# Kernel tuning notes

Hardware: AMD Instinct MI355X
Metric: run time of the kernel (lower is better)

The kernel has to match this reference:

```python
import jax, jax.numpy as jnp
import numpy as np

G, N, E, D, K = 32, 512, 8192, 256, 2048
LAMB_EDGE = 1.0
LAMB_NODE = 0.0
CODEBOOK_WEIGHT = 1000.0
ALPHA = 100.0


def setup_inputs() -> dict:
    key = jax.random.key(0)
    ks = jax.random.split(key, 12)
    s = 1.0 / np.sqrt(D)
    return {
        'feats': jax.random.normal(ks[0], (G, N, D), jnp.float32),
        'src': jax.random.randint(ks[1], (G, E), 0, N, jnp.int32),
        'dst': jax.random.randint(ks[2], (G, E), 0, N, jnp.int32),
        'W1': jax.random.normal(ks[3], (D, D), jnp.float32) * s,
        'b1': jnp.zeros((D,), jnp.float32),
        'W2': jax.random.normal(ks[4], (D, D), jnp.float32) * s,
        'b2': jnp.zeros((D,), jnp.float32),
        'ln_gamma': jnp.ones((D,), jnp.float32),
        'ln_beta': jnp.zeros((D,), jnp.float32),
        'dec1_W': jax.random.normal(ks[5], (D, D), jnp.float32) * s,
        'dec1_b': jnp.zeros((D,), jnp.float32),
        'dec2_W': jax.random.normal(ks[6], (D, D), jnp.float32) * s,
        'dec2_b': jnp.zeros((D,), jnp.float32),
        'codebook': jax.random.normal(ks[7], (K, D), jnp.float32),
    }


def _graph_conv(x, src, dst, W, b):
    # DGL GraphConv, norm='both': D_out^{-1/2} -> sum aggregate -> D_in^{-1/2} -> linear -> relu
    ones_e = jnp.ones(src.shape[0], x.dtype)
    deg_out = jnp.clip(jax.ops.segment_sum(ones_e, src, num_segments=N), 1.0)
    deg_in = jnp.clip(jax.ops.segment_sum(ones_e, dst, num_segments=N), 1.0)
    h = x * jax.lax.rsqrt(deg_out)[:, None]
    m = jax.ops.segment_sum(h[src], dst, num_segments=N)
    m = m * jax.lax.rsqrt(deg_in)[:, None]
    return jax.nn.relu(m @ W + b)


def _layernorm(x, gamma, beta):
    mu = jnp.mean(x, axis=-1, keepdims=True)
    var = jnp.mean(jnp.square(x - mu), axis=-1, keepdims=True)
    return (x - mu) * jax.lax.rsqrt(var + 1e-5) * gamma + beta


def _edge_loss(qe, src, dst):
    # qe: [N, D] decoded node embeddings for one graph
    logits = qe @ qe.T  # [N, N]
    adj = jnp.zeros((N, N), qe.dtype).at[src, dst].set(1.0)
    mask = jnp.triu(jnp.ones((N, N), bool), k=1)
    num_possible = N * N / 2.0
    num_edges = jnp.sum(jnp.where(mask, adj, 0.0))
    pos_weight = (num_possible - num_edges) / (num_edges + 1e-6)
    # BCEWithLogits with pos_weight, mean over strict upper triangle
    per = pos_weight * adj * jax.nn.softplus(-logits) + (1.0 - adj) * jax.nn.softplus(logits)
    return jnp.sum(jnp.where(mask, per, 0.0)) / (N * (N - 1) / 2.0)


def reference(feats, src, dst, W1, b1, W2, b2, ln_gamma, ln_beta,
              dec1_W, dec1_b, dec2_W, dec2_b, codebook):
    conv = jax.vmap(_graph_conv, in_axes=(0, 0, 0, None, None))
    h1 = conv(feats, src, dst, W1, b1)              # [G, N, D]
    h1 = _layernorm(h1, ln_gamma, ln_beta)           # dropout eval = identity
    h2 = conv(h1, src, dst, W2, b2)                  # [G, N, D]

    hf = h2.reshape(G * N, D)
    # cosine-sim VQ
    xn = hf * jax.lax.rsqrt(jnp.sum(hf * hf, -1, keepdims=True) + 1e-12)
    cn = codebook * jax.lax.rsqrt(jnp.sum(codebook * codebook, -1, keepdims=True) + 1e-12)
    dist = xn @ cn.T                                 # [G*N, K] cosine similarities
    idx = jnp.argmax(dist, axis=-1)
    q = codebook[idx]
    q_st = hf + jax.lax.stop_gradient(q - hf)        # straight-through
    vq_loss = CODEBOOK_WEIGHT * jnp.mean(jnp.square(q - jax.lax.stop_gradient(hf)))

    quantized_edge = (q_st @ dec1_W + dec1_b).reshape(G, N, D)
    quantized_node = q_st @ dec2_W + dec2_b

    edge_losses = jax.vmap(_edge_loss)(quantized_edge, src, dst)  # [G]
    edge_rec_loss = LAMB_EDGE * jnp.mean(edge_losses)
    feature_rec_loss = LAMB_NODE * jnp.mean(jnp.square(hf - quantized_node))
    loss = feature_rec_loss + edge_rec_loss * ALPHA + vq_loss
    return loss
```

## Files before the change

### kernel.cpp

```cpp
#include <hip/hip_runtime.h>
#include <math.h>

#define G 32
#define N 512
#define E 8192
#define D 256
#define KCB 2048
#define GN (G * N)

typedef __bf16 bf16x8 __attribute__((ext_vector_type(8)));
typedef float f32x4 __attribute__((ext_vector_type(4)));

static const size_t OFF_SPOS   = 0;
static const size_t OFF_SNEG   = OFF_SPOS + 256;
static const size_t OFF_BEST   = OFF_SNEG + 256;
static const size_t ZERO_BYTES = OFF_BEST + (size_t)GN * 8;
static const size_t OFF_NEDGE  = ZERO_BYTES;
static const size_t OFF_VQPART = OFF_NEDGE + 256;
static const size_t OFF_ROWOFF = OFF_VQPART + (size_t)GN * 4;
static const size_t OFF_RS_OUT = OFF_ROWOFF + (size_t)GN * 4;
static const size_t OFF_RS_IN  = OFF_RS_OUT + (size_t)GN * 4;
static const size_t OFF_DEG_IN = OFF_RS_IN + (size_t)GN * 4;
static const size_t OFF_CSR    = OFF_DEG_IN + (size_t)GN * 4;
static const size_t OFF_ADJ    = OFF_CSR + (size_t)G * E * 4;
static const size_t OFF_RNC    = OFF_ADJ + (size_t)G * N * N / 8;
static const size_t OFF_W1T    = OFF_RNC + (size_t)KCB * 4;
static const size_t OFF_W2T    = OFF_W1T + (size_t)D * D * 2;
static const size_t OFF_DWT    = OFF_W2T + (size_t)D * D * 2;
static const size_t OFF_CBB    = OFF_DWT + (size_t)D * D * 2;
static const size_t OFF_FEB    = OFF_CBB + (size_t)KCB * D * 2;
static const size_t OFF_AGGB   = OFF_FEB + (size_t)GN * D * 2;
static const size_t OFF_BF32   = OFF_AGGB + (size_t)GN * D * 2;
static const size_t OFF_BCB    = OFF_BF32 + (size_t)GN * D * 4;

__global__ void __launch_bounds__(512) k_graph_build(
    const int* __restrict__ src, const int* __restrict__ dst,
    unsigned* __restrict__ adj, int* __restrict__ nedge, int* __restrict__ row_off_g,
    float* __restrict__ rs_in_g, float* __restrict__ rs_out_g,
    int* __restrict__ deg_in_g, int* __restrict__ csr_src) {
  int g = blockIdx.x, t = threadIdx.x;
  __shared__ unsigned s_adj[N * N / 32];
  __shared__ int s_deg_in[N], s_deg_out[N];
  __shared__ int s_buf[2][N];
  __shared__ int s_red[8];
  for (int i = t; i < N * N / 32; i += 512) s_adj[i] = 0;
  s_deg_in[t] = 0;
  s_deg_out[t] = 0;
  __syncthreads();
  const int* sg = src + g * E;
  const int* dg = dst + g * E;
  int se[E / 512], de[E / 512];
  int ecount = 0;
#pragma unroll
  for (int j = 0; j < E / 512; ++j) {
    int s = sg[t + j * 512], d = dg[t + j * 512];
    se[j] = s; de[j] = d;
    atomicAdd(&s_deg_out[s], 1);
    atomicAdd(&s_deg_in[d], 1);
    if (s < d) {
      int bit = s * N + d;
      unsigned m = 1u << (bit & 31);
      unsigned old = atomicOr(&s_adj[bit >> 5], m);
      if (!(old & m)) ++ecount;
    }
  }
  __syncthreads();
  for (int off = 32; off; off >>= 1) ecount += __shfl_down(ecount, off);
  if ((t & 63) == 0) s_red[t >> 6] = ecount;
  __syncthreads();
  if (t == 0) {
    int tot = 0;
    for (int i = 0; i < 8; ++i) tot += s_red[i];
    nedge[g] = tot;
  }
  unsigned* adjg = adj + (size_t)g * (N * N / 32);
  for (int i = t; i < N * N / 32; i += 512) adjg[i] = s_adj[i];
  int own = s_deg_in[t];
  s_buf[0][t] = own;
  __syncthreads();
  int cur = 0;
  for (int off = 1; off < N; off <<= 1) {
    int v = s_buf[cur][t];
    if (t >= off) v += s_buf[cur][t - off];
    s_buf[cur ^ 1][t] = v;
    __syncthreads();
    cur ^= 1;
  }
  int roff = s_buf[cur][t] - own;
  row_off_g[g * N + t] = roff;
  deg_in_g[g * N + t] = own;
  rs_in_g[g * N + t] = rsqrtf(fmaxf((float)own, 1.0f));
  rs_out_g[g * N + t] = rsqrtf(fmaxf((float)s_deg_out[t], 1.0f));
  __syncthreads();
  s_deg_in[t] = roff;
  __syncthreads();
  int* csrg = csr_src + g * E;
#pragma unroll
  for (int j = 0; j < E / 512; ++j) {
    int slot = atomicAdd(&s_deg_in[de[j]], 1);
    csrg[slot] = se[j];
  }
}

__global__ void __launch_bounds__(256) k_prep_w(
    const float* __restrict__ W1, const float* __restrict__ W2,
    const float* __restrict__ dW, __bf16* __restrict__ W1t,
    __bf16* __restrict__ W2t, __bf16* __restrict__ dWt) {
  __shared__ float tile[32][33];
  const float* in = blockIdx.z == 0 ? W1 : (blockIdx.z == 1 ? W2 : dW);
  __bf16* out = blockIdx.z == 0 ? W1t : (blockIdx.z == 1 ? W2t : dWt);
  int bx = blockIdx.x * 32, by = blockIdx.y * 32;
  int tx = threadIdx.x & 31, ty = threadIdx.x >> 5;
#pragma unroll
  for (int r = 0; r < 32; r += 8) tile[ty + r][tx] = in[(by + ty + r) * D + bx + tx];
  __syncthreads();
#pragma unroll
  for (int r = 0; r < 32; r += 8)
    out[(size_t)(bx + ty + r) * D + by + tx] = (__bf16)tile[tx][ty + r];
}

__global__ void k_prep_cb(const float* __restrict__ cb, __bf16* __restrict__ cbb,
                          float* __restrict__ rnc) {
  int row = blockIdx.x, t = threadIdx.x;
  float v = cb[(size_t)row * D + t];
  cbb[(size_t)row * D + t] = (__bf16)v;
  float s2 = v * v;
  for (int off = 32; off; off >>= 1) s2 += __shfl_down(s2, off);
  __shared__ float w[4];
  if ((t & 63) == 0) w[t >> 6] = s2;
  __syncthreads();
  if (t == 0) rnc[row] = rsqrtf(w[0] + w[1] + w[2] + w[3] + 1e-12f);
}

__global__ void k_cast_feats(const float* __restrict__ x, unsigned* __restrict__ xb2) {
  int i = blockIdx.x * 256 + threadIdx.x;
  float2 v = ((const float2*)x)[i];
  union { __bf16 h[2]; unsigned u; } o;
  o.h[0] = (__bf16)v.x; o.h[1] = (__bf16)v.y;
  xb2[i] = o.u;
}

__global__ void __launch_bounds__(128) k_aggregate(
    const unsigned* __restrict__ x2, const int* __restrict__ csr_src,
    const int* __restrict__ row_off, const int* __restrict__ deg_in,
    const float* __restrict__ rs_in, const float* __restrict__ rs_out,
    unsigned* __restrict__ out2) {
  int b = blockIdx.x;
  int g = ((b & 7) << 2) | (b >> 12);
  int n = (b >> 3) & 511;
  int gn = (g << 9) | n;
  int t = threadIdx.x;
  int cnt = deg_in[gn];
  int base = g * E + row_off[gn];
  __shared__ int sidx[128];
  __shared__ float sw[128];
  float ax = 0.f, ay = 0.f;
  for (int c0 = 0; c0 < cnt; c0 += 128) {
    int m = min(128, cnt - c0);
    if (t < m) {
      int s = csr_src[base + c0 + t];
      sidx[t] = s;
      sw[t] = rs_out[(g << 9) | s];
    }
    __syncthreads();
    for (int j = 0; j < m; ++j) {
      int s = sidx[j];
      float w = sw[j];
      unsigned v = x2[((size_t)((g << 9) | s) << 7) + t];
      ax += __uint_as_float(v << 16) * w;
      ay += __uint_as_float(v & 0xffff0000u) * w;
    }
    __syncthreads();
  }
  float ri = rs_in[gn];
  union { __bf16 h[2]; unsigned u; } o;
  o.h[0] = (__bf16)(ax * ri); o.h[1] = (__bf16)(ay * ri);
  out2[((size_t)gn << 7) + t] = o.u;
}

__device__ __forceinline__ void gload_lds16(const __bf16* g, __bf16* s) {
  __builtin_amdgcn_global_load_lds((const __attribute__((address_space(1))) void*)g,
                                   (__attribute__((address_space(3))) void*)s, 16, 0, 0);
}

__device__ __forceinline__ void mfma_core(const __bf16* __restrict__ Abase,
                                          const __bf16* __restrict__ Bbase,
                                          __bf16* sA, __bf16* sB, f32x4 (&acc)[4][4],
                                          int tid) {
  int wave = tid >> 6, lane = tid & 63;
  int wr = (wave >> 1) * 64, wc = (wave & 1) * 64;
  int m = lane & 15, quad = lane >> 4;
  for (int k0 = 0; k0 < 256; k0 += 32) {
#pragma unroll
    for (int c2 = 0; c2 < 2; ++c2) {
      int c = wave * 2 + c2;
      int row = c * 16 + (lane >> 2);
      int col = (lane & 3) * 8;
      gload_lds16(Abase + (size_t)row * 256 + k0 + col, sA + c * 512);
      gload_lds16(Bbase + (size_t)row * 256 + k0 + col, sB + c * 512);
    }
    __syncthreads();
    bf16x8 af[4], bfr[4];
#pragma unroll
    for (int i = 0; i < 4; ++i) {
      af[i] = *(const bf16x8*)&sA[(wr + i * 16 + m) * 32 + quad * 8];
      bfr[i] = *(const bf16x8*)&sB[(wc + i * 16 + m) * 32 + quad * 8];
    }
#pragma unroll
    for (int i = 0; i < 4; ++i)
#pragma unroll
      for (int j = 0; j < 4; ++j)
        acc[i][j] = __builtin_amdgcn_mfma_f32_16x16x32_bf16(af[i], bfr[j], acc[i][j], 0, 0, 0);
    __syncthreads();
  }
}

template <bool RELU, bool SF32, bool SBF16>
__global__ void __launch_bounds__(256) k_gemm_bf16(
    const __bf16* __restrict__ A, const __bf16* __restrict__ Bt,
    const float* __restrict__ bias, float* __restrict__ C, __bf16* __restrict__ Cb) {
  __shared__ __align__(16) __bf16 sA[4096], sB[4096];
  f32x4 acc[4][4] = {};
  int tid = threadIdx.x;
  int row0 = blockIdx.x * 128, col0 = blockIdx.y * 128;
  mfma_core(A + (size_t)row0 * 256, Bt + (size_t)col0 * 256, sA, sB, acc, tid);
  int wave = tid >> 6, lane = tid & 63;
  int wr = (wave >> 1) * 64, wc = (wave & 1) * 64, quad = lane >> 4, n16 = lane & 15;
#pragma unroll
  for (int j = 0; j < 4; ++j) {
    int col = col0 + wc + j * 16 + n16;
    float bs = bias[col];
#pragma unroll
    for (int i = 0; i < 4; ++i)
#pragma unroll
      for (int r = 0; r < 4; ++r) {
        int row = row0 + wr + i * 16 + quad * 4 + r;
        float v = acc[i][j][r] + bs;
        if (RELU) v = fmaxf(v, 0.f);
        if (SF32) C[(size_t)row * 256 + col] = v;
        if (SBF16) Cb[(size_t)row * 256 + col] = (__bf16)v;
      }
  }
}

__global__ void __launch_bounds__(128) k_layernorm(
    const float* __restrict__ x, unsigned* __restrict__ outb2,
    const float* __restrict__ gamma, const float* __restrict__ beta) {
  int row = blockIdx.x, t = threadIdx.x;
  float2 v = ((const float2*)x)[row * 128 + t];
  float s = v.x + v.y, s2 = v.x * v.x + v.y * v.y;
  for (int off = 32; off; off >>= 1) {
    s += __shfl_down(s, off);
    s2 += __shfl_down(s2, off);
  }
  __shared__ float w1[2], w2[2];
  if ((t & 63) == 0) { w1[t >> 6] = s; w2[t >> 6] = s2; }
  __syncthreads();
  float mu = (w1[0] + w1[1]) * (1.f / D);
  float m2 = (w2[0] + w2[1]) * (1.f / D);
  float rstd = rsqrtf(m2 - mu * mu + 1e-5f);
  float2 gm = ((const float2*)gamma)[t];
  float2 bt = ((const float2*)beta)[t];
  union { __bf16 h[2]; unsigned u; } o;
  o.h[0] = (__bf16)((v.x - mu) * rstd * gm.x + bt.x);
  o.h[1] = (__bf16)((v.y - mu) * rstd * gm.y + bt.y);
  outb2[row * 128 + t] = o.u;
}

__global__ void __launch_bounds__(256) k_vq_bf16(
    const __bf16* __restrict__ A, const __bf16* __restrict__ CBt,
    const float* __restrict__ rnc, unsigned long long* __restrict__ best) {
  __shared__ __align__(16) __bf16 sA[4096], sB[4096];
  f32x4 acc[4][4] = {};
  int tid = threadIdx.x;
  int row0 = blockIdx.x * 128, col0 = blockIdx.y * 128;
  mfma_core(A + (size_t)row0 * 256, CBt + (size_t)col0 * 256, sA, sB, acc, tid);
  int wave = tid >> 6, lane = tid & 63;
  int wr = (wave >> 1) * 64, wc = (wave & 1) * 64, quad = lane >> 4, n16 = lane & 15;
#pragma unroll
  for (int i = 0; i < 4; ++i) {
    unsigned long long cand[4] = {0ull, 0ull, 0ull, 0ull};
#pragma unroll
    for (int j = 0; j < 4; ++j) {
      int col = col0 + wc + j * 16 + n16;
      float rc = rnc[col];
#pragma unroll
      for (int r = 0; r < 4; ++r) {
        float sim = acc[i][j][r] * rc;
        unsigned u = __float_as_uint(sim);
        u = ((int)u >= 0) ? (u | 0x80000000u) : ~u;
        unsigned long long c64 =
            ((unsigned long long)u << 32) | (0xFFFFFFFFu - (unsigned)col);
        cand[r] = cand[r] > c64 ? cand[r] : c64;
      }
    }
#pragma unroll
    for (int off = 1; off < 16; off <<= 1)
#pragma unroll
      for (int r = 0; r < 4; ++r) {
        unsigned long long o = __shfl_xor(cand[r], off, 64);
        cand[r] = cand[r] > o ? cand[r] : o;
      }
    if (n16 == 0)
#pragma unroll
      for (int r = 0; r < 4; ++r)
        atomicMax(&best[row0 + wr + i * 16 + quad * 4 + r], cand[r]);
  }
}

__global__ void k_vq_gather(const unsigned long long* __restrict__ best,
                            const float* __restrict__ cb, const __bf16* __restrict__ cbb,
                            const float* __restrict__ hf, __bf16* __restrict__ qb,
                            float* __restrict__ vq_part) {
  int row = blockIdx.x, t = threadIdx.x;
  unsigned long long b = best[row];
  int c = (int)(0xFFFFFFFFu - (unsigned)(b & 0xFFFFFFFFull));
  qb[(size_t)row * D + t] = cbb[(size_t)c * D + t];
  float d = cb[(size_t)c * D + t] - hf[(size_t)row * D + t];
  float s2 = d * d;
  for (int off = 32; off; off >>= 1) s2 += __shfl_down(s2, off);
  __shared__ float w[4];
  if ((t & 63) == 0) w[t >> 6] = s2;
  __syncthreads();
  if (t == 0) vq_part[row] = w[0] + w[1] + w[2] + w[3];
}

__constant__ int c_ti[10] = {0, 0, 0, 0, 1, 1, 1, 2, 2, 3};
__constant__ int c_tj[10] = {0, 1, 2, 3, 1, 2, 3, 2, 3, 3};

__global__ void __launch_bounds__(256) k_edge_bf16(
    const __bf16* __restrict__ qe, const unsigned* __restrict__ adj,
    float* __restrict__ Spos, float* __restrict__ Sneg) {
  int g = blockIdx.x / 10, p = blockIdx.x % 10;
  int row0 = c_ti[p] * 128, col0 = c_tj[p] * 128;
  const __bf16* Ag = qe + (size_t)g * N * D;
  const unsigned* adjg = adj + (size_t)g * (N * N / 32);
  __shared__ __align__(16) __bf16 sA[4096], sB[4096];
  f32x4 acc[4][4] = {};
  int tid = threadIdx.x;
  mfma_core(Ag + (size_t)row0 * 256, Ag + (size_t)col0 * 256, sA, sB, acc, tid);
  int wave = tid >> 6, lane = tid & 63;
  int wr = (wave >> 1) * 64, wc = (wave & 1) * 64, quad = lane >> 4, n16 = lane & 15;
  float spos = 0.f, sneg = 0.f;
#pragma unroll
  for (int i = 0; i < 4; ++i)
#pragma unroll
    for (int j = 0; j < 4; ++j) {
      int c = col0 + wc + j * 16 + n16;
#pragma unroll
      for (int r = 0; r < 4; ++r) {
        int rr = row0 + wr + i * 16 + quad * 4 + r;
        if (rr < c) {
          float l = acc[i][j][r];
          int bit = rr * N + c;
          bool a = (adjg[bit >> 5] >> (bit & 31)) & 1u;
          float spabs = log1pf(expf(-fabsf(l)));
          if (a) spos += fmaxf(-l, 0.f) + spabs;
          else sneg += fmaxf(l, 0.f) + spabs;
        }
      }
    }
  for (int off = 32; off; off >>= 1) {
    spos += __shfl_down(spos, off);
    sneg += __shfl_down(sneg, off);
  }
  __shared__ float wp[4], wn[4];
  if ((tid & 63) == 0) { wp[tid >> 6] = spos; wn[tid >> 6] = sneg; }
  __syncthreads();
  if (tid == 0) {
    atomicAdd(&Spos[g], wp[0] + wp[1] + wp[2] + wp[3]);
    atomicAdd(&Sneg[g], wn[0] + wn[1] + wn[2] + wn[3]);
  }
}

__global__ void __launch_bounds__(256) k_final(
    const int* __restrict__ nedge, const float* __restrict__ Spos,
    const float* __restrict__ Sneg, const float* __restrict__ vq_part,
    float* __restrict__ out) {
  int t = threadIdx.x;
  float vq = 0.f;
  for (int i = t; i < GN; i += 256) vq += vq_part[i];
  float el = 0.f;
  if (t < G) {
    float ne = (float)nedge[t];
    float pw = (131072.0f - ne) / (ne + 1e-6f);
    el = (pw * Spos[t] + Sneg[t]) * (1.0f / 130816.0f);
  }
  for (int off = 32; off; off >>= 1) {
    vq += __shfl_down(vq, off);
    el += __shfl_down(el, off);
  }
  __shared__ float wv[4], we[4];
  if ((t & 63) == 0) { wv[t >> 6] = vq; we[t >> 6] = el; }
  __syncthreads();
  if (t == 0) {
    float vqs = wv[0] + wv[1] + wv[2] + wv[3];
    float els = we[0] + we[1] + we[2] + we[3];
    out[0] = 100.0f * (els * (1.0f / G)) + 1000.0f * (vqs * (1.0f / ((float)GN * D)));
  }
}

extern "C" void kernel_launch(void* const* d_in, const int* in_sizes, int n_in,
                              void* d_out, int out_size, void* d_ws, size_t ws_size,
                              hipStream_t stream) {
  const float* feats = (const float*)d_in[0];
  const int* src = (const int*)d_in[1];
  const int* dst = (const int*)d_in[2];
  const float* W1 = (const float*)d_in[3];
  const float* b1 = (const float*)d_in[4];
  const float* W2 = (const float*)d_in[5];
  const float* b2 = (const float*)d_in[6];
  const float* ln_g = (const float*)d_in[7];
  const float* ln_b = (const float*)d_in[8];
  const float* dec1_W = (const float*)d_in[9];
  const float* dec1_b = (const float*)d_in[10];
  const float* cb = (const float*)d_in[13];

  char* ws = (char*)d_ws;
  float* Spos = (float*)(ws + OFF_SPOS);
  float* Sneg = (float*)(ws + OFF_SNEG);
  unsigned long long* best = (unsigned long long*)(ws + OFF_BEST);
  int* nedge = (int*)(ws + OFF_NEDGE);
  float* vq_part = (float*)(ws + OFF_VQPART);
  int* row_off = (int*)(ws + OFF_ROWOFF);
  float* rs_out = (float*)(ws + OFF_RS_OUT);
  float* rs_in = (float*)(ws + OFF_RS_IN);
  int* deg_in = (int*)(ws + OFF_DEG_IN);
  int* csr_src = (int*)(ws + OFF_CSR);
  unsigned* adj = (unsigned*)(ws + OFF_ADJ);
  float* rnc = (float*)(ws + OFF_RNC);
  __bf16* W1t = (__bf16*)(ws + OFF_W1T);
  __bf16* W2t = (__bf16*)(ws + OFF_W2T);
  __bf16* dWt = (__bf16*)(ws + OFF_DWT);
  __bf16* cbb = (__bf16*)(ws + OFF_CBB);
  unsigned* featsb2 = (unsigned*)(ws + OFF_FEB);
  __bf16* aggb = (__bf16*)(ws + OFF_AGGB);
  unsigned* aggb2 = (unsigned*)(ws + OFF_AGGB);
  float* bf32 = (float*)(ws + OFF_BF32);
  __bf16* bcb = (__bf16*)(ws + OFF_BCB);
  unsigned* bcb2 = (unsigned*)(ws + OFF_BCB);

  hipMemsetAsync(d_ws, 0, ZERO_BYTES, stream);

  k_graph_build<<<G, 512, 0, stream>>>(src, dst, adj, nedge, row_off, rs_in, rs_out,
                                       deg_in, csr_src);
  k_prep_w<<<dim3(8, 8, 3), 256, 0, stream>>>(W1, W2, dec1_W, W1t, W2t, dWt);
  k_prep_cb<<<KCB, D, 0, stream>>>(cb, cbb, rnc);
  k_cast_feats<<<GN * D / 512, 256, 0, stream>>>(feats, featsb2);

  k_aggregate<<<GN, 128, 0, stream>>>(featsb2, csr_src, row_off, deg_in, rs_in, rs_out,
                                      aggb2);
  k_gemm_bf16<true, true, false><<<dim3(GN / 128, 2), 256, 0, stream>>>(
      aggb, W1t, b1, bf32, nullptr);
  k_layernorm<<<GN, 128, 0, stream>>>(bf32, bcb2, ln_g, ln_b);

  k_aggregate<<<GN, 128, 0, stream>>>(bcb2, csr_src, row_off, deg_in, rs_in, rs_out, aggb2);
  k_gemm_bf16<true, true, true><<<dim3(GN / 128, 2), 256, 0, stream>>>(
      aggb, W2t, b2, bf32, bcb);

  k_vq_bf16<<<dim3(GN / 128, KCB / 128), 256, 0, stream>>>(bcb, cbb, rnc, best);
  k_vq_gather<<<GN, 256, 0, stream>>>(best, cb, cbb, bf32, bcb, vq_part);

  k_gemm_bf16<false, false, true><<<dim3(GN / 128, 2), 256, 0, stream>>>(
      bcb, dWt, dec1_b, nullptr, aggb);
  k_edge_bf16<<<10 * G, 256, 0, stream>>>(aggb, adj, Spos, Sneg);

  k_final<<<1, 256, 0, stream>>>(nedge, Spos, Sneg, vq_part, (float*)d_out);
}
```

Baseline: 278.1 us.

## Split graph build across blocks, fuse prep kernels, drop feature cast pass

Graph construction moves from one 512-thread block per graph to three kernels (degree/adjacency via global atomics over 256 blocks, a per-graph scan, and a CSR scatter), so more of the GPU works on it. The weight and codebook prep kernels merge into one launch. The separate fp32-to-bf16 feature cast is removed by having the first aggregation read fp32 directly. The first GEMM now writes bf16 only, and layernorm works in place on bf16, which cuts fp32 traffic. The costs are a larger memset for the adjacency and degree buffers, global atomic contention, and layernorm statistics computed from bf16-rounded inputs.

```diff
diff --git a/kernel.cpp b/kernel.cpp
--- a/kernel.cpp
+++ b/kernel.cpp
@@ -11,137 +11,135 @@
 typedef __bf16 bf16x8 __attribute__((ext_vector_type(8)));
 typedef float f32x4 __attribute__((ext_vector_type(4)));
 
-static const size_t OFF_SPOS   = 0;
-static const size_t OFF_SNEG   = OFF_SPOS + 256;
-static const size_t OFF_BEST   = OFF_SNEG + 256;
-static const size_t ZERO_BYTES = OFF_BEST + (size_t)GN * 8;
-static const size_t OFF_NEDGE  = ZERO_BYTES;
-static const size_t OFF_VQPART = OFF_NEDGE + 256;
-static const size_t OFF_ROWOFF = OFF_VQPART + (size_t)GN * 4;
-static const size_t OFF_RS_OUT = OFF_ROWOFF + (size_t)GN * 4;
-static const size_t OFF_RS_IN  = OFF_RS_OUT + (size_t)GN * 4;
-static const size_t OFF_DEG_IN = OFF_RS_IN + (size_t)GN * 4;
-static const size_t OFF_CSR    = OFF_DEG_IN + (size_t)GN * 4;
-static const size_t OFF_ADJ    = OFF_CSR + (size_t)G * E * 4;
-static const size_t OFF_RNC    = OFF_ADJ + (size_t)G * N * N / 8;
-static const size_t OFF_W1T    = OFF_RNC + (size_t)KCB * 4;
-static const size_t OFF_W2T    = OFF_W1T + (size_t)D * D * 2;
-static const size_t OFF_DWT    = OFF_W2T + (size_t)D * D * 2;
-static const size_t OFF_CBB    = OFF_DWT + (size_t)D * D * 2;
-static const size_t OFF_FEB    = OFF_CBB + (size_t)KCB * D * 2;
-static const size_t OFF_AGGB   = OFF_FEB + (size_t)GN * D * 2;
-static const size_t OFF_BF32   = OFF_AGGB + (size_t)GN * D * 2;
-static const size_t OFF_BCB    = OFF_BF32 + (size_t)GN * D * 4;
-
-__global__ void __launch_bounds__(512) k_graph_build(
+static const size_t OFF_SPOS    = 0;
+static const size_t OFF_SNEG    = OFF_SPOS + 256;
+static const size_t OFF_NEDGE   = OFF_SNEG + 256;
+static const size_t OFF_BEST    = OFF_NEDGE + 256;
+static const size_t OFF_DEG_OUT = OFF_BEST + (size_t)GN * 8;
+static const size_t OFF_DEG_IN  = OFF_DEG_OUT + (size_t)GN * 4;
+static const size_t OFF_CURSOR  = OFF_DEG_IN + (size_t)GN * 4;
+static const size_t OFF_ADJ     = OFF_CURSOR + (size_t)GN * 4;
+static const size_t ZERO_BYTES  = OFF_ADJ + (size_t)G * N * N / 8;
+static const size_t OFF_VQPART  = ZERO_BYTES;
+static const size_t OFF_ROWOFF  = OFF_VQPART + (size_t)GN * 4;
+static const size_t OFF_RS_OUT  = OFF_ROWOFF + (size_t)GN * 4;
+static const size_t OFF_RS_IN   = OFF_RS_OUT + (size_t)GN * 4;
+static const size_t OFF_CSR     = OFF_RS_IN + (size_t)GN * 4;
+static const size_t OFF_RNC     = OFF_CSR + (size_t)G * E * 4;
+static const size_t OFF_W1T     = OFF_RNC + (size_t)KCB * 4;
+static const size_t OFF_W2T     = OFF_W1T + (size_t)D * D * 2;
+static const size_t OFF_DWT     = OFF_W2T + (size_t)D * D * 2;
+static const size_t OFF_CBB     = OFF_DWT + (size_t)D * D * 2;
+static const size_t OFF_AGGB    = OFF_CBB + (size_t)KCB * D * 2;
+static const size_t OFF_BF32    = OFF_AGGB + (size_t)GN * D * 2;
+static const size_t OFF_BCB     = OFF_BF32 + (size_t)GN * D * 4;
+
+__global__ void __launch_bounds__(256) k_build_deg(
     const int* __restrict__ src, const int* __restrict__ dst,
-    unsigned* __restrict__ adj, int* __restrict__ nedge, int* __restrict__ row_off_g,
-    float* __restrict__ rs_in_g, float* __restrict__ rs_out_g,
-    int* __restrict__ deg_in_g, int* __restrict__ csr_src) {
-  int g = blockIdx.x, t = threadIdx.x;
-  __shared__ unsigned s_adj[N * N / 32];
-  __shared__ int s_deg_in[N], s_deg_out[N];
-  __shared__ int s_buf[2][N];
-  __shared__ int s_red[8];
-  for (int i = t; i < N * N / 32; i += 512) s_adj[i] = 0;
-  s_deg_in[t] = 0;
-  s_deg_out[t] = 0;
-  __syncthreads();
+    int* __restrict__ deg_out, int* __restrict__ deg_in,
+    unsigned* __restrict__ adj, int* __restrict__ nedge) {
+  int b = blockIdx.x;
+  int g = b >> 3;
+  int e0 = (b & 7) << 10;
+  int t = threadIdx.x;
   const int* sg = src + g * E;
   const int* dg = dst + g * E;
-  int se[E / 512], de[E / 512];
   int ecount = 0;
 #pragma unroll
-  for (int j = 0; j < E / 512; ++j) {
-    int s = sg[t + j * 512], d = dg[t + j * 512];
-    se[j] = s; de[j] = d;
-    atomicAdd(&s_deg_out[s], 1);
-    atomicAdd(&s_deg_in[d], 1);
+  for (int j = 0; j < 4; ++j) {
+    int idx = e0 + j * 256 + t;
+    int s = sg[idx], d = dg[idx];
+    atomicAdd(&deg_out[(g << 9) | s], 1);
+    atomicAdd(&deg_in[(g << 9) | d], 1);
     if (s < d) {
       int bit = s * N + d;
       unsigned m = 1u << (bit & 31);
-      unsigned old = atomicOr(&s_adj[bit >> 5], m);
+      unsigned old = atomicOr(&adj[g * (N * N / 32) + (bit >> 5)], m);
       if (!(old & m)) ++ecount;
     }
   }
-  __syncthreads();
   for (int off = 32; off; off >>= 1) ecount += __shfl_down(ecount, off);
-  if ((t & 63) == 0) s_red[t >> 6] = ecount;
-  __syncthreads();
-  if (t == 0) {
-    int tot = 0;
-    for (int i = 0; i < 8; ++i) tot += s_red[i];
-    nedge[g] = tot;
-  }
-  unsigned* adjg = adj + (size_t)g * (N * N / 32);
-  for (int i = t; i < N * N / 32; i += 512) adjg[i] = s_adj[i];
-  int own = s_deg_in[t];
-  s_buf[0][t] = own;
+  __shared__ int sred[4];
+  if ((t & 63) == 0) sred[t >> 6] = ecount;
+  __syncthreads();
+  if (t == 0) atomicAdd(&nedge[g], sred[0] + sred[1] + sred[2] + sred[3]);
+}
+
+__global__ void __launch_bounds__(512) k_build_scan(
+    const int* __restrict__ deg_in, const int* __restrict__ deg_out,
+    int* __restrict__ row_off, float* __restrict__ rs_in, float* __restrict__ rs_out) {
+  int g = blockIdx.x, t = threadIdx.x;
+  __shared__ int buf[2][N];
+  int own = deg_in[(g << 9) | t];
+  buf[0][t] = own;
   __syncthreads();
   int cur = 0;
   for (int off = 1; off < N; off <<= 1) {
-    int v = s_buf[cur][t];
-    if (t >= off) v += s_buf[cur][t - off];
-    s_buf[cur ^ 1][t] = v;
+    int v = buf[cur][t];
+    if (t >= off) v += buf[cur][t - off];
+    buf[cur ^ 1][t] = v;
     __syncthreads();
     cur ^= 1;
   }
-  int roff = s_buf[cur][t] - own;
-  row_off_g[g * N + t] = roff;
-  deg_in_g[g * N + t] = own;
-  rs_in_g[g * N + t] = rsqrtf(fmaxf((float)own, 1.0f));
-  rs_out_g[g * N + t] = rsqrtf(fmaxf((float)s_deg_out[t], 1.0f));
-  __syncthreads();
-  s_deg_in[t] = roff;
-  __syncthreads();
-  int* csrg = csr_src + g * E;
-#pragma unroll
-  for (int j = 0; j < E / 512; ++j) {
-    int slot = atomicAdd(&s_deg_in[de[j]], 1);
-    csrg[slot] = se[j];
-  }
-}
-
-__global__ void __launch_bounds__(256) k_prep_w(
+  row_off[(g << 9) | t] = buf[cur][t] - own;
+  rs_in[(g << 9) | t] = rsqrtf(fmaxf((float)own, 1.0f));
+  rs_out[(g << 9) | t] = rsqrtf(fmaxf((float)deg_out[(g << 9) | t], 1.0f));
+}
+
+__global__ void __launch_bounds__(256) k_build_scatter(
+    const int* __restrict__ src, const int* __restrict__ dst,
+    const int* __restrict__ row_off, int* __restrict__ cursor, int* __restrict__ csr_src) {
+  int b = blockIdx.x;
+  int g = b >> 3;
+  int e0 = (b & 7) << 10;
+  int t = threadIdx.x;
+  const int* sg = src + g * E;
+  const int* dg = dst + g * E;
+#pragma unroll
+  for (int j = 0; j < 4; ++j) {
+    int idx = e0 + j * 256 + t;
+    int s = sg[idx], d = dg[idx];
+    int gn = (g << 9) | d;
+    int slot = atomicAdd(&cursor[gn], 1);
+    csr_src[g * E + row_off[gn] + slot] = s;
+  }
+}
+
+__global__ void __launch_bounds__(256) k_prep(
     const float* __restrict__ W1, const float* __restrict__ W2,
     const float* __restrict__ dW, __bf16* __restrict__ W1t,
-    __bf16* __restrict__ W2t, __bf16* __restrict__ dWt) {
-  __shared__ float tile[32][33];
-  const float* in = blockIdx.z == 0 ? W1 : (blockIdx.z == 1 ? W2 : dW);
-  __bf16* out = blockIdx.z == 0 ? W1t : (blockIdx.z == 1 ? W2t : dWt);
-  int bx = blockIdx.x * 32, by = blockIdx.y * 32;
-  int tx = threadIdx.x & 31, ty = threadIdx.x >> 5;
-#pragma unroll
-  for (int r = 0; r < 32; r += 8) tile[ty + r][tx] = in[(by + ty + r) * D + bx + tx];
-  __syncthreads();
-#pragma unroll
-  for (int r = 0; r < 32; r += 8)
-    out[(size_t)(bx + ty + r) * D + by + tx] = (__bf16)tile[tx][ty + r];
-}
-
-__global__ void k_prep_cb(const float* __restrict__ cb, __bf16* __restrict__ cbb,
-                          float* __restrict__ rnc) {
-  int row = blockIdx.x, t = threadIdx.x;
-  float v = cb[(size_t)row * D + t];
-  cbb[(size_t)row * D + t] = (__bf16)v;
-  float s2 = v * v;
-  for (int off = 32; off; off >>= 1) s2 += __shfl_down(s2, off);
-  __shared__ float w[4];
-  if ((t & 63) == 0) w[t >> 6] = s2;
-  __syncthreads();
-  if (t == 0) rnc[row] = rsqrtf(w[0] + w[1] + w[2] + w[3] + 1e-12f);
-}
-
-__global__ void k_cast_feats(const float* __restrict__ x, unsigned* __restrict__ xb2) {
-  int i = blockIdx.x * 256 + threadIdx.x;
-  float2 v = ((const float2*)x)[i];
-  union { __bf16 h[2]; unsigned u; } o;
-  o.h[0] = (__bf16)v.x; o.h[1] = (__bf16)v.y;
-  xb2[i] = o.u;
-}
-
+    __bf16* __restrict__ W2t, __bf16* __restrict__ dWt,
+    const float* __restrict__ cb, __bf16* __restrict__ cbb, float* __restrict__ rnc) {
+  int b = blockIdx.x;
+  if (b < 192) {
+    __shared__ float tile[32][33];
+    int z = b / 64, tt = b % 64;
+    int bx = (tt & 7) * 32, by = (tt >> 3) * 32;
+    const float* in = z == 0 ? W1 : (z == 1 ? W2 : dW);
+    __bf16* out = z == 0 ? W1t : (z == 1 ? W2t : dWt);
+    int tx = threadIdx.x & 31, ty = threadIdx.x >> 5;
+#pragma unroll
+    for (int r = 0; r < 32; r += 8) tile[ty + r][tx] = in[(by + ty + r) * D + bx + tx];
+    __syncthreads();
+#pragma unroll
+    for (int r = 0; r < 32; r += 8)
+      out[(size_t)(bx + ty + r) * D + by + tx] = (__bf16)tile[tx][ty + r];
+  } else {
+    int row = b - 192, t = threadIdx.x;
+    float v = cb[(size_t)row * D + t];
+    cbb[(size_t)row * D + t] = (__bf16)v;
+    float s2 = v * v;
+    for (int off = 32; off; off >>= 1) s2 += __shfl_down(s2, off);
+    __shared__ float w[4];
+    if ((t & 63) == 0) w[t >> 6] = s2;
+    __syncthreads();
+    if (t == 0) rnc[row] = rsqrtf(w[0] + w[1] + w[2] + w[3] + 1e-12f);
+  }
+}
+
+template <bool FP32IN>
 __global__ void __launch_bounds__(128) k_aggregate(
-    const unsigned* __restrict__ x2, const int* __restrict__ csr_src,
+    const void* __restrict__ xin, const int* __restrict__ csr_src,
     const int* __restrict__ row_off, const int* __restrict__ deg_in,
     const float* __restrict__ rs_in, const float* __restrict__ rs_out,
     unsigned* __restrict__ out2) {
@@ -166,15 +164,23 @@
     for (int j = 0; j < m; ++j) {
       int s = sidx[j];
       float w = sw[j];
-      unsigned v = x2[((size_t)((g << 9) | s) << 7) + t];
-      ax += __uint_as_float(v << 16) * w;
-      ay += __uint_as_float(v & 0xffff0000u) * w;
+      size_t ridx = ((size_t)((g << 9) | s) << 7) + t;
+      if (FP32IN) {
+        float2 v = ((const float2*)xin)[ridx];
+        ax += v.x * w;
+        ay += v.y * w;
+      } else {
+        unsigned v = ((const unsigned*)xin)[ridx];
+        ax += __uint_as_float(v << 16) * w;
+        ay += __uint_as_float(v & 0xffff0000u) * w;
+      }
     }
     __syncthreads();
   }
   float ri = rs_in[gn];
   union { __bf16 h[2]; unsigned u; } o;
-  o.h[0] = (__bf16)(ax * ri); o.h[1] = (__bf16)(ay * ri);
+  o.h[0] = (__bf16)(ax * ri);
+  o.h[1] = (__bf16)(ay * ri);
   out2[((size_t)gn << 7) + t] = o.u;
 }
 
@@ -244,11 +250,12 @@
 }
 
 __global__ void __launch_bounds__(128) k_layernorm(
-    const float* __restrict__ x, unsigned* __restrict__ outb2,
-    const float* __restrict__ gamma, const float* __restrict__ beta) {
+    unsigned* __restrict__ xb2, const float* __restrict__ gamma,
+    const float* __restrict__ beta) {
   int row = blockIdx.x, t = threadIdx.x;
-  float2 v = ((const float2*)x)[row * 128 + t];
-  float s = v.x + v.y, s2 = v.x * v.x + v.y * v.y;
+  unsigned u = xb2[row * 128 + t];
+  float vx = __uint_as_float(u << 16), vy = __uint_as_float(u & 0xffff0000u);
+  float s = vx + vy, s2 = vx * vx + vy * vy;
   for (int off = 32; off; off >>= 1) {
     s += __shfl_down(s, off);
     s2 += __shfl_down(s2, off);
@@ -262,9 +269,9 @@
   float2 gm = ((const float2*)gamma)[t];
   float2 bt = ((const float2*)beta)[t];
   union { __bf16 h[2]; unsigned u; } o;
-  o.h[0] = (__bf16)((v.x - mu) * rstd * gm.x + bt.x);
-  o.h[1] = (__bf16)((v.y - mu) * rstd * gm.y + bt.y);
-  outb2[row * 128 + t] = o.u;
+  o.h[0] = (__bf16)((vx - mu) * rstd * gm.x + bt.x);
+  o.h[1] = (__bf16)((vy - mu) * rstd * gm.y + bt.y);
+  xb2[row * 128 + t] = o.u;
 }
 
 __global__ void __launch_bounds__(256) k_vq_bf16(
@@ -419,21 +426,22 @@
   char* ws = (char*)d_ws;
   float* Spos = (float*)(ws + OFF_SPOS);
   float* Sneg = (float*)(ws + OFF_SNEG);
+  int* nedge = (int*)(ws + OFF_NEDGE);
   unsigned long long* best = (unsigned long long*)(ws + OFF_BEST);
-  int* nedge = (int*)(ws + OFF_NEDGE);
+  int* deg_out = (int*)(ws + OFF_DEG_OUT);
+  int* deg_in = (int*)(ws + OFF_DEG_IN);
+  int* cursor = (int*)(ws + OFF_CURSOR);
+  unsigned* adj = (unsigned*)(ws + OFF_ADJ);
   float* vq_part = (float*)(ws + OFF_VQPART);
   int* row_off = (int*)(ws + OFF_ROWOFF);
   float* rs_out = (float*)(ws + OFF_RS_OUT);
   float* rs_in = (float*)(ws + OFF_RS_IN);
-  int* deg_in = (int*)(ws + OFF_DEG_IN);
   int* csr_src = (int*)(ws + OFF_CSR);
-  unsigned* adj = (unsigned*)(ws + OFF_ADJ);
   float* rnc = (float*)(ws + OFF_RNC);
   __bf16* W1t = (__bf16*)(ws + OFF_W1T);
   __bf16* W2t = (__bf16*)(ws + OFF_W2T);
   __bf16* dWt = (__bf16*)(ws + OFF_DWT);
   __bf16* cbb = (__bf16*)(ws + OFF_CBB);
-  unsigned* featsb2 = (unsigned*)(ws + OFF_FEB);
   __bf16* aggb = (__bf16*)(ws + OFF_AGGB);
   unsigned* aggb2 = (unsigned*)(ws + OFF_AGGB);
   float* bf32 = (float*)(ws + OFF_BF32);
@@ -442,19 +450,19 @@
 
   hipMemsetAsync(d_ws, 0, ZERO_BYTES, stream);
 
-  k_graph_build<<<G, 512, 0, stream>>>(src, dst, adj, nedge, row_off, rs_in, rs_out,
-                                       deg_in, csr_src);
-  k_prep_w<<<dim3(8, 8, 3), 256, 0, stream>>>(W1, W2, dec1_W, W1t, W2t, dWt);
-  k_prep_cb<<<KCB, D, 0, stream>>>(cb, cbb, rnc);
-  k_cast_feats<<<GN * D / 512, 256, 0, stream>>>(feats, featsb2);
-
-  k_aggregate<<<GN, 128, 0, stream>>>(featsb2, csr_src, row_off, deg_in, rs_in, rs_out,
-                                      aggb2);
-  k_gemm_bf16<true, true, false><<<dim3(GN / 128, 2), 256, 0, stream>>>(
-      aggb, W1t, b1, bf32, nullptr);
-  k_layernorm<<<GN, 128, 0, stream>>>(bf32, bcb2, ln_g, ln_b);
-
-  k_aggregate<<<GN, 128, 0, stream>>>(bcb2, csr_src, row_off, deg_in, rs_in, rs_out, aggb2);
+  k_build_deg<<<256, 256, 0, stream>>>(src, dst, deg_out, deg_in, adj, nedge);
+  k_build_scan<<<G, 512, 0, stream>>>(deg_in, deg_out, row_off, rs_in, rs_out);
+  k_build_scatter<<<256, 256, 0, stream>>>(src, dst, row_off, cursor, csr_src);
+  k_prep<<<192 + KCB, 256, 0, stream>>>(W1, W2, dec1_W, W1t, W2t, dWt, cb, cbb, rnc);
+
+  k_aggregate<true><<<GN, 128, 0, stream>>>(feats, csr_src, row_off, deg_in, rs_in,
+                                            rs_out, aggb2);
+  k_gemm_bf16<true, false, true><<<dim3(GN / 128, 2), 256, 0, stream>>>(
+      aggb, W1t, b1, nullptr, bcb);
+  k_layernorm<<<GN, 128, 0, stream>>>(bcb2, ln_g, ln_b);
+
+  k_aggregate<false><<<GN, 128, 0, stream>>>(bcb2, csr_src, row_off, deg_in, rs_in,
+                                             rs_out, aggb2);
   k_gemm_bf16<true, true, true><<<dim3(GN / 128, 2), 256, 0, stream>>>(
       aggb, W2t, b2, bf32, bcb);
 
```

Result: slower. 295.6 us (+6.3%).
